# Performance work log

Measured on AMD Instinct MI355X. Metric: run time of the kernel, lower is better.

The kernel has to match this reference:

```python
import jax, jax.numpy as jnp
import numpy as np

N = 4096   # nodes
D = 512    # feature dim
E = 65536  # edges
HOPS = 10  # APPNP K (init arg 'hops')
ALPHA = 0.5


def setup_inputs() -> dict:
    key = jax.random.key(0)
    k1, k2, k3 = jax.random.split(key, 3)
    x_train = jax.random.normal(k1, (N, D), dtype=jnp.float32)
    # kernel_scale = nn.Linear(D, 1, bias=False) weight, flattened to [D]
    w = jax.random.normal(k2, (D,), dtype=jnp.float32) * 0.05
    edge_index = jax.random.randint(k3, (2, E), 0, N, dtype=jnp.int32)
    return {"x_train": x_train, "w": w, "edge_index": edge_index}


def appnp(x0, src, dst, hops, alpha):
    # torch_geometric APPNP with gcn_norm (add self-loops, symmetric norm), dropout=0
    n = x0.shape[0]
    loop = jnp.arange(n, dtype=src.dtype)
    s = jnp.concatenate([src, loop])
    d = jnp.concatenate([dst, loop])
    deg = jax.ops.segment_sum(jnp.ones_like(s, dtype=x0.dtype), d, num_segments=n)
    dis = deg ** -0.5  # deg >= 1 thanks to self-loops
    norm = dis[s] * dis[d]

    def body(h, _):
        agg = jax.ops.segment_sum(norm[:, None] * h[s], d, num_segments=n)
        return (1.0 - alpha) * agg + alpha * x0, None

    h, _ = jax.lax.scan(body, x0, None, length=hops)
    return h


def reference(x_train, w, edge_index):
    n = x_train.shape[0]
    # RBF_kernel: K[i,j] = sum_d w_d * (x_i - x_j)_d^2 for i != j, diag = 1 (the eye)
    xw = x_train * w                                   # [N, D]
    sq = jnp.sum(xw * x_train, axis=1)                 # [N] weighted squared norms
    K = sq[:, None] + sq[None, :] - 2.0 * (xw @ x_train.T)  # [N, N]
    idx = jnp.arange(n)
    K = K.at[idx, idx].set(1.0)

    src, dst = edge_index[0], edge_index[1]
    kgg = appnp(K, src, dst, HOPS, ALPHA)
    kgg = appnp(kgg.T, src, dst, HOPS, ALPHA)

    # adj = dense coo(edge_index, ones); diag = (diag(adj.sum(dim=1)) + 1) ** -0.5
    # (adds 1 to the WHOLE matrix, so off-diagonal entries become 1.0 -- faithful)
    deg_row = jax.ops.segment_sum(jnp.ones((edge_index.shape[1],), K.dtype), src, num_segments=n)
    Dmat = (jnp.diag(deg_row) + 1.0) ** -0.5           # [N, N]
    kgg = Dmat * kgg       # elementwise, as in the original
    kgg = Dmat * kgg.T
    return kgg
```

## Files before the change

### kernel.cpp

```cpp
#include <hip/hip_runtime.h>
#include <stdint.h>

#define Nn 4096
#define Dd 512
#define Ee 65536
#define HOPS 10
#define TPB 512
#define RPT (Nn / TPB)
#define CT 4
#define WCAP 64
#define BCOLS 1028
#define KEXT 1536

typedef unsigned short ushortT;
typedef short bf16x8 __attribute__((ext_vector_type(8)));
typedef float f32x4 __attribute__((ext_vector_type(4)));

__device__ __forceinline__ unsigned short bf16r(float x) {
  unsigned int b = __float_as_uint(x);
  return (unsigned short)((b + 0x7FFFu + ((b >> 16) & 1u)) >> 16);
}
__device__ __forceinline__ float ubf(unsigned short h) {
  return __uint_as_float(((unsigned int)h) << 16);
}
__device__ __forceinline__ void gld16(const unsigned short* g, unsigned short* lds) {
  __builtin_amdgcn_global_load_lds(
      (const __attribute__((address_space(1))) unsigned int*)g,
      (__attribute__((address_space(3))) unsigned int*)lds, 16, 0, 0);
}

__global__ __launch_bounds__(256) void k_sq(const float* __restrict__ x,
                                            const float* __restrict__ w,
                                            float* __restrict__ sq) {
  int row = blockIdx.x;
  int tid = threadIdx.x;
  const float* xr = x + (size_t)row * Dd;
  float partial = 0.f;
  for (int d = tid; d < Dd; d += 256) {
    float xv = xr[d];
    partial += xv * xv * w[d];
  }
  for (int off = 32; off >= 1; off >>= 1) partial += __shfl_down(partial, off, 64);
  __shared__ float red[4];
  int wv = tid >> 6, ln = tid & 63;
  if (ln == 0) red[wv] = partial;
  __syncthreads();
  if (tid == 0) sq[row] = red[0] + red[1] + red[2] + red[3];
}

__global__ void k_count(const int* __restrict__ src, const int* __restrict__ dst,
                        int* __restrict__ degi, int* __restrict__ degrow) {
  int e = blockIdx.x * blockDim.x + threadIdx.x;
  if (e < Ee) {
    atomicAdd(&degi[dst[e]], 1);
    atomicAdd(&degrow[src[e]], 1);
  }
}

__global__ void k_dis(const int* __restrict__ degi, const int* __restrict__ degrow,
                      float* __restrict__ dis, float* __restrict__ d2) {
  int i = blockIdx.x * 256 + threadIdx.x;
  dis[i] = rsqrtf((float)(degi[i] + 1));
  d2[i] = 1.0f / ((float)degrow[i] + 1.0f);
}

__global__ void k_hist(const int* __restrict__ degi, int* __restrict__ binbase) {
  __shared__ int h[WCAP + 1];
  int t = threadIdx.x;
  if (t <= WCAP) h[t] = 0;
  __syncthreads();
  for (int i = t; i < Nn; i += 256) {
    int d = degi[i] + 1;
    if (d > WCAP) d = WCAP;
    atomicAdd(&h[d], 1);
  }
  __syncthreads();
  if (t == 0) {
    int run = 0;
    for (int b = 0; b <= WCAP; b++) { int c = h[b]; binbase[b] = run; run += c; }
  }
}

__global__ void k_scatter(const int* __restrict__ degi, const int* __restrict__ binbase,
                          int* __restrict__ bincnt, int* __restrict__ perm,
                          int* __restrict__ rnk) {
  int i = blockIdx.x * 256 + threadIdx.x;
  int d = degi[i] + 1;
  if (d > WCAP) d = WCAP;
  int pos = binbase[d] + atomicAdd(&bincnt[d], 1);
  perm[pos] = i;
  rnk[i] = pos;
}

__global__ void k_wsub(const int* __restrict__ degi, const int* __restrict__ perm,
                       int* __restrict__ wsub) {
  int t = threadIdx.x;
  int d = degi[perm[t * 64 + 63]] + 1;
  wsub[t] = d > WCAP ? WCAP : d;
}

__global__ void k_fill_ell(const int* __restrict__ src, const int* __restrict__ dst,
                           const float* __restrict__ dis, const int* __restrict__ rnk,
                           int* __restrict__ slot, int2* __restrict__ ell) {
  int i = blockIdx.x * blockDim.x + threadIdx.x;
  if (i < Ee) {
    int s = src[i], d = dst[i];
    int p = atomicAdd(&slot[d], 1);
    if (p < WCAP) ell[(size_t)p * Nn + rnk[d]] = make_int2(s, __float_as_int(dis[s] * dis[d]));
  } else if (i < Ee + Nn) {
    int v = i - Ee;
    int p = atomicAdd(&slot[v], 1);
    if (p < WCAP) ell[(size_t)p * Nn + rnk[v]] = make_int2(v, __float_as_int(dis[v] * dis[v]));
  }
}

__global__ __launch_bounds__(256) void k_xpose(const float* __restrict__ x,
                                               const float* __restrict__ w,
                                               float* __restrict__ xcat) {
  __shared__ float tile[32][33];
  int cx = blockIdx.x, rx = blockIdx.y;
  int t = threadIdx.x, txc = t & 31, tyc = t >> 5;
#pragma unroll
  for (int i = 0; i < 4; i++) {
    int a = tyc + i * 8;
    tile[a][txc] = x[(size_t)(rx * 32 + a) * Dd + cx * 32 + txc];
  }
  __syncthreads();
#pragma unroll
  for (int i = 0; i < 4; i++) {
    int a = tyc + i * 8;
    int c = cx * 32 + a;
    float v = tile[txc][a];
    xcat[(size_t)c * Nn + rx * 32 + txc] = -2.0f * w[c] * v;
    xcat[(size_t)(512 + c) * Nn + rx * 32 + txc] = v;
  }
}

__global__ void k_tail(const float* __restrict__ sq, float* __restrict__ xcat) {
  int r = blockIdx.x * 256 + threadIdx.x;
  xcat[(size_t)1024 * Nn + r] = sq[r];
  xcat[(size_t)1025 * Nn + r] = 1.0f;
  xcat[(size_t)1026 * Nn + r] = 0.0f;
  xcat[(size_t)1027 * Nn + r] = 0.0f;
}

template <int MODE>
__global__ __launch_bounds__(TPB, 4) void k_appnp(const float* __restrict__ xsrc,
                                                  unsigned short* __restrict__ mb,
                                                  unsigned short* __restrict__ aext,
                                                  unsigned short* __restrict__ bext,
                                                  float* __restrict__ mu,
                                                  float* __restrict__ m1,
                                                  const int2* __restrict__ ell,
                                                  const int* __restrict__ perm,
                                                  const int* __restrict__ wsub) {
  extern __shared__ float4 h4[];
  int j0 = blockIdx.x * CT;
  int tid = threadIdx.x;
  int wv = tid >> 6, ln = tid & 63;
  int qb = wv * 512 + ln;

#pragma unroll
  for (int rr = 0; rr < RPT; rr++) {
    int r = tid + rr * TPB;
    float4 v;
    if (MODE == 1) {
      v.x = (r == j0 + 0) ? 1.f : 0.f;
      v.y = (r == j0 + 1) ? 1.f : 0.f;
      v.z = (r == j0 + 2) ? 1.f : 0.f;
      v.w = (r == j0 + 3) ? 1.f : 0.f;
    } else {
      v.x = xsrc[(size_t)(j0 + 0) * Nn + r];
      v.y = xsrc[(size_t)(j0 + 1) * Nn + r];
      v.z = xsrc[(size_t)(j0 + 2) * Nn + r];
      v.w = xsrc[(size_t)(j0 + 3) * Nn + r];
    }
    h4[r] = v;
  }

  int ws[RPT];
#pragma unroll
  for (int rr = 0; rr < RPT; rr++)
    ws[rr] = __builtin_amdgcn_readfirstlane(wsub[wv * 8 + rr]);
  const int Wv = ws[RPT - 1];

  int rp[RPT];
#pragma unroll
  for (int rr = 0; rr < RPT; rr++) rp[rr] = perm[qb + rr * 64];

  __syncthreads();
  float4 x0r[RPT];
#pragma unroll
  for (int rr = 0; rr < RPT; rr++) x0r[rr] = h4[rp[rr]];

  float4 acc[RPT];
  for (int it = 0; it < HOPS; it++) {
    int2 cur[RPT];
#pragma unroll
    for (int rr = 0; rr < RPT; rr++) cur[rr] = ell[qb + rr * 64];
#pragma unroll
    for (int rr = 0; rr < RPT; rr++) acc[rr] = x0r[rr];
    for (int s = 0; s < Wv; s++) {
      int sn = s + 1;
      int2 nxt[RPT];
#pragma unroll
      for (int rr = 0; rr < RPT; rr++)
        if (sn < ws[rr]) nxt[rr] = ell[(size_t)sn * Nn + qb + rr * 64];
#pragma unroll
      for (int rr = 0; rr < RPT; rr++)
        if (s < ws[rr]) {
          float vv = __int_as_float(cur[rr].y);
          float4 hu = h4[cur[rr].x];
          acc[rr].x = fmaf(vv, hu.x, acc[rr].x);
          acc[rr].y = fmaf(vv, hu.y, acc[rr].y);
          acc[rr].z = fmaf(vv, hu.z, acc[rr].z);
          acc[rr].w = fmaf(vv, hu.w, acc[rr].w);
        }
#pragma unroll
      for (int rr = 0; rr < RPT; rr++)
        if (sn < ws[rr]) cur[rr] = nxt[rr];
    }
#pragma unroll
    for (int rr = 0; rr < RPT; rr++) {
      acc[rr].x *= 0.5f; acc[rr].y *= 0.5f; acc[rr].z *= 0.5f; acc[rr].w *= 0.5f;
    }
    __syncthreads();
#pragma unroll
    for (int rr = 0; rr < RPT; rr++) h4[rp[rr]] = acc[rr];
    __syncthreads();
  }

  if (MODE == 1) {
#pragma unroll
    for (int rr = 0; rr < RPT; rr++) {
      int r = tid + rr * TPB;
      float4 a = h4[r];
      ushort4 o = make_ushort4(bf16r(a.x), bf16r(a.y), bf16r(a.z), bf16r(a.w));
      *(ushort4*)&mb[(size_t)r * Nn + j0] = o;
    }
  } else {
    if (j0 < 1024) {
#pragma unroll
      for (int rr = 0; rr < RPT; rr++) {
        int r = tid + rr * TPB;
        float4 a = h4[r];
        ushort4 hi = make_ushort4(bf16r(a.x), bf16r(a.y), bf16r(a.z), bf16r(a.w));
        ushort4 lo = make_ushort4(bf16r(a.x - ubf(hi.x)), bf16r(a.y - ubf(hi.y)),
                                  bf16r(a.z - ubf(hi.z)), bf16r(a.w - ubf(hi.w)));
        if (j0 < 512) {
          *(ushort4*)&aext[(size_t)r * KEXT + j0] = hi;
          *(ushort4*)&aext[(size_t)r * KEXT + 512 + j0] = hi;
          *(ushort4*)&aext[(size_t)r * KEXT + 1024 + j0] = lo;
        } else {
          int c = j0 - 512;
          *(ushort4*)&bext[(size_t)r * KEXT + c] = hi;
          *(ushort4*)&bext[(size_t)r * KEXT + 512 + c] = lo;
          *(ushort4*)&bext[(size_t)r * KEXT + 1024 + c] = hi;
        }
      }
    } else if (j0 == 1024) {
#pragma unroll
      for (int rr = 0; rr < RPT; rr++) {
        int r = tid + rr * TPB;
        float4 a = h4[r];
        mu[r] = a.x;
        m1[r] = a.y;
      }
    }
  }
}

__device__ __forceinline__ void mm_step(const unsigned short* __restrict__ Ap, int lda,
                                        const unsigned short* __restrict__ Bp, int ldb,
                                        unsigned short* As, unsigned short* Bs,
                                        int i0, int j0, int k0, int l, int w, int wr,
                                        int wc, f32x4 acc[4][4]) {
#pragma unroll
  for (int j = 0; j < 2; j++) {
    int row = (w * 2 + j) * 16 + (l >> 2);
    int clog = (l & 3) ^ ((row >> 1) & 3);
    gld16(Ap + (size_t)(i0 + row) * lda + k0 + clog * 8, As + (w * 2 + j) * 512);
    gld16(Bp + (size_t)(j0 + row) * ldb + k0 + clog * 8, Bs + (w * 2 + j) * 512);
  }
  __syncthreads();
  bf16x8 af[4], bg[4];
#pragma unroll
  for (int m = 0; m < 4; m++) {
    int ar = wr * 64 + m * 16 + (l & 15);
    af[m] = *(const bf16x8*)(As + ar * 32 + (((l >> 4) ^ ((ar >> 1) & 3))) * 8);
    int br = wc * 64 + m * 16 + (l & 15);
    bg[m] = *(const bf16x8*)(Bs + br * 32 + (((l >> 4) ^ ((br >> 1) & 3))) * 8);
  }
#pragma unroll
  for (int m = 0; m < 4; m++)
#pragma unroll
    for (int n = 0; n < 4; n++)
      acc[m][n] = __builtin_amdgcn_mfma_f32_16x16x32_bf16(af[m], bg[n], acc[m][n], 0, 0, 0);
  __syncthreads();
}

__global__ __launch_bounds__(256) void k_mm(const unsigned short* __restrict__ Mb,
                                            const unsigned short* __restrict__ Aext,
                                            const unsigned short* __restrict__ Bext,
                                            const float* __restrict__ mu,
                                            const float* __restrict__ m1,
                                            const float* __restrict__ d2,
                                            float* __restrict__ out) {
  __shared__ unsigned short As[128 * 32];
  __shared__ unsigned short Bs[128 * 32];
  int i0 = blockIdx.y * 128, j0 = blockIdx.x * 128;
  int tid = threadIdx.x, l = tid & 63, w = tid >> 6;
  int wr = w >> 1, wc = w & 1;
  f32x4 acc[4][4];
#pragma unroll
  for (int m = 0; m < 4; m++)
#pragma unroll
    for (int n = 0; n < 4; n++) acc[m][n] = (f32x4){0.f, 0.f, 0.f, 0.f};

  for (int k0 = 0; k0 < Nn; k0 += 32)
    mm_step(Mb, Nn, Mb, Nn, As, Bs, i0, j0, k0, l, w, wr, wc, acc);
  for (int k0 = 0; k0 < KEXT; k0 += 32)
    mm_step(Aext, KEXT, Bext, KEXT, As, Bs, i0, j0, k0, l, w, wr, wc, acc);

#pragma unroll
  for (int m = 0; m < 4; m++) {
#pragma unroll
    for (int n = 0; n < 4; n++) {
#pragma unroll
      for (int q = 0; q < 4; q++) {
        int gi = i0 + wr * 64 + m * 16 + ((l >> 4) << 2) + q;
        int gj = j0 + wc * 64 + n * 16 + (l & 15);
        float v = acc[m][n][q] + mu[gi] * m1[gj] + m1[gi] * mu[gj];
        if (gi == gj) v *= d2[gi];
        out[(size_t)gi * Nn + gj] = v;
      }
    }
  }
}

extern "C" void kernel_launch(void* const* d_in, const int* in_sizes, int n_in,
                              void* d_out, int out_size, void* d_ws, size_t ws_size,
                              hipStream_t stream) {
  const float* x = (const float*)d_in[0];
  const float* w = (const float*)d_in[1];
  const int* ei = (const int*)d_in[2];
  const int* src = ei;
  const int* dstv = ei + Ee;
  float* out = (float*)d_out;

  unsigned short* Mb = (unsigned short*)d_ws;
  float* xcat = (float*)d_ws;
  unsigned short* aext = (unsigned short*)((char*)d_ws + (size_t)Nn * Nn * 2);
  unsigned short* bext = aext + (size_t)Nn * KEXT;
  int2* ell = (int2*)(bext + (size_t)Nn * KEXT);
  float* sq = (float*)(ell + (size_t)WCAP * Nn);
  float* dis = sq + Nn;
  float* d2 = dis + Nn;
  float* mu = d2 + Nn;
  float* m1 = mu + Nn;
  int* degi = (int*)(m1 + Nn);
  int* degrow = degi + Nn;
  int* slotcnt = degrow + Nn;
  int* bincnt = slotcnt + Nn;
  int* binbase = bincnt + (WCAP + 1);
  int* perm = binbase + (WCAP + 1);
  int* rnk = perm + Nn;
  int* wsub = rnk + Nn;

  hipMemsetAsync(ell, 0, (size_t)WCAP * Nn * sizeof(int2), stream);
  hipMemsetAsync(degi, 0, sizeof(int) * (3 * Nn + (WCAP + 1)), stream);

  k_sq<<<Nn, 256, 0, stream>>>(x, w, sq);
  k_count<<<Ee / 256, 256, 0, stream>>>(src, dstv, degi, degrow);
  k_dis<<<Nn / 256, 256, 0, stream>>>(degi, degrow, dis, d2);
  k_hist<<<1, 256, 0, stream>>>(degi, binbase);
  k_scatter<<<Nn / 256, 256, 0, stream>>>(degi, binbase, bincnt, perm, rnk);
  k_wsub<<<1, 64, 0, stream>>>(degi, perm, wsub);
  k_fill_ell<<<(Ee + Nn + 255) / 256, 256, 0, stream>>>(src, dstv, dis, rnk, slotcnt, ell);
  k_xpose<<<dim3(16, 128), 256, 0, stream>>>(x, w, xcat);
  k_tail<<<Nn / 256, 256, 0, stream>>>(sq, xcat);

  k_appnp<0><<<BCOLS / CT, TPB, Nn * sizeof(float4), stream>>>(xcat, nullptr, aext, bext, mu,
                                                               m1, ell, perm, wsub);
  k_appnp<1><<<Nn / CT, TPB, Nn * sizeof(float4), stream>>>(nullptr, Mb, nullptr, nullptr,
                                                            nullptr, nullptr, ell, perm, wsub);
  k_mm<<<dim3(Nn / 128, Nn / 128), 256, 0, stream>>>(Mb, aext, bext, mu, m1, d2, out);
}
```

Baseline: 1.041 ms.

## Propagate x once and apply weights after APPNP; widen GEMM K-tile and swizzle blocks

The APPNP propagation is linear, so propagating the -2*w*x columns is replaced by propagating x alone and scaling by -2*w after propagation. This halves the number of feature columns diffused (516 instead of 1028). The final GEMM also moves from a K-step of 32 to 64 with a new XOR-swizzled LDS layout, which halves the number of barriers per K. Block indices are remapped so neighbouring workgroups share tiles in cache. The cost is more LDS per block (32KB), which may lower occupancy, and slightly different rounding from scaling after propagation.

```diff
diff --git a/kernel.cpp b/kernel.cpp
--- a/kernel.cpp
+++ b/kernel.cpp
@@ -9,10 +9,9 @@
 #define RPT (Nn / TPB)
 #define CT 4
 #define WCAP 64
-#define BCOLS 1028
+#define BCOLS 516
 #define KEXT 1536
 
-typedef unsigned short ushortT;
 typedef short bf16x8 __attribute__((ext_vector_type(8)));
 typedef float f32x4 __attribute__((ext_vector_type(4)));
 
@@ -115,7 +114,6 @@
 }
 
 __global__ __launch_bounds__(256) void k_xpose(const float* __restrict__ x,
-                                               const float* __restrict__ w,
                                                float* __restrict__ xcat) {
   __shared__ float tile[32][33];
   int cx = blockIdx.x, rx = blockIdx.y;
@@ -130,22 +128,21 @@
   for (int i = 0; i < 4; i++) {
     int a = tyc + i * 8;
     int c = cx * 32 + a;
-    float v = tile[txc][a];
-    xcat[(size_t)c * Nn + rx * 32 + txc] = -2.0f * w[c] * v;
-    xcat[(size_t)(512 + c) * Nn + rx * 32 + txc] = v;
+    xcat[(size_t)c * Nn + rx * 32 + txc] = tile[txc][a];
   }
 }
 
 __global__ void k_tail(const float* __restrict__ sq, float* __restrict__ xcat) {
   int r = blockIdx.x * 256 + threadIdx.x;
-  xcat[(size_t)1024 * Nn + r] = sq[r];
-  xcat[(size_t)1025 * Nn + r] = 1.0f;
-  xcat[(size_t)1026 * Nn + r] = 0.0f;
-  xcat[(size_t)1027 * Nn + r] = 0.0f;
+  xcat[(size_t)512 * Nn + r] = sq[r];
+  xcat[(size_t)513 * Nn + r] = 1.0f;
+  xcat[(size_t)514 * Nn + r] = 0.0f;
+  xcat[(size_t)515 * Nn + r] = 0.0f;
 }
 
 template <int MODE>
 __global__ __launch_bounds__(TPB, 4) void k_appnp(const float* __restrict__ xsrc,
+                                                  const float* __restrict__ wp,
                                                   unsigned short* __restrict__ mb,
                                                   unsigned short* __restrict__ aext,
                                                   unsigned short* __restrict__ bext,
@@ -239,26 +236,28 @@
       *(ushort4*)&mb[(size_t)r * Nn + j0] = o;
     }
   } else {
-    if (j0 < 1024) {
+    if (j0 < 512) {
+      float w0 = -2.f * wp[j0 + 0], w1 = -2.f * wp[j0 + 1];
+      float w2 = -2.f * wp[j0 + 2], w3 = -2.f * wp[j0 + 3];
 #pragma unroll
       for (int rr = 0; rr < RPT; rr++) {
         int r = tid + rr * TPB;
         float4 a = h4[r];
-        ushort4 hi = make_ushort4(bf16r(a.x), bf16r(a.y), bf16r(a.z), bf16r(a.w));
-        ushort4 lo = make_ushort4(bf16r(a.x - ubf(hi.x)), bf16r(a.y - ubf(hi.y)),
-                                  bf16r(a.z - ubf(hi.z)), bf16r(a.w - ubf(hi.w)));
-        if (j0 < 512) {
-          *(ushort4*)&aext[(size_t)r * KEXT + j0] = hi;
-          *(ushort4*)&aext[(size_t)r * KEXT + 512 + j0] = hi;
-          *(ushort4*)&aext[(size_t)r * KEXT + 1024 + j0] = lo;
-        } else {
-          int c = j0 - 512;
-          *(ushort4*)&bext[(size_t)r * KEXT + c] = hi;
-          *(ushort4*)&bext[(size_t)r * KEXT + 512 + c] = lo;
-          *(ushort4*)&bext[(size_t)r * KEXT + 1024 + c] = hi;
-        }
+        ushort4 yhi = make_ushort4(bf16r(a.x), bf16r(a.y), bf16r(a.z), bf16r(a.w));
+        ushort4 ylo = make_ushort4(bf16r(a.x - ubf(yhi.x)), bf16r(a.y - ubf(yhi.y)),
+                                   bf16r(a.z - ubf(yhi.z)), bf16r(a.w - ubf(yhi.w)));
+        float4 p = make_float4(w0 * a.x, w1 * a.y, w2 * a.z, w3 * a.w);
+        ushort4 phi = make_ushort4(bf16r(p.x), bf16r(p.y), bf16r(p.z), bf16r(p.w));
+        ushort4 plo = make_ushort4(bf16r(p.x - ubf(phi.x)), bf16r(p.y - ubf(phi.y)),
+                                   bf16r(p.z - ubf(phi.z)), bf16r(p.w - ubf(phi.w)));
+        *(ushort4*)&bext[(size_t)r * KEXT + j0] = yhi;
+        *(ushort4*)&bext[(size_t)r * KEXT + 512 + j0] = ylo;
+        *(ushort4*)&bext[(size_t)r * KEXT + 1024 + j0] = yhi;
+        *(ushort4*)&aext[(size_t)r * KEXT + j0] = phi;
+        *(ushort4*)&aext[(size_t)r * KEXT + 512 + j0] = phi;
+        *(ushort4*)&aext[(size_t)r * KEXT + 1024 + j0] = plo;
       }
-    } else if (j0 == 1024) {
+    } else if (j0 == 512) {
 #pragma unroll
       for (int rr = 0; rr < RPT; rr++) {
         int r = tid + rr * TPB;
@@ -275,27 +274,31 @@
                                         unsigned short* As, unsigned short* Bs,
                                         int i0, int j0, int k0, int l, int w, int wr,
                                         int wc, f32x4 acc[4][4]) {
-#pragma unroll
-  for (int j = 0; j < 2; j++) {
-    int row = (w * 2 + j) * 16 + (l >> 2);
-    int clog = (l & 3) ^ ((row >> 1) & 3);
-    gld16(Ap + (size_t)(i0 + row) * lda + k0 + clog * 8, As + (w * 2 + j) * 512);
-    gld16(Bp + (size_t)(j0 + row) * ldb + k0 + clog * 8, Bs + (w * 2 + j) * 512);
-  }
-  __syncthreads();
-  bf16x8 af[4], bg[4];
-#pragma unroll
-  for (int m = 0; m < 4; m++) {
-    int ar = wr * 64 + m * 16 + (l & 15);
-    af[m] = *(const bf16x8*)(As + ar * 32 + (((l >> 4) ^ ((ar >> 1) & 3))) * 8);
-    int br = wc * 64 + m * 16 + (l & 15);
-    bg[m] = *(const bf16x8*)(Bs + br * 32 + (((l >> 4) ^ ((br >> 1) & 3))) * 8);
-  }
-#pragma unroll
-  for (int m = 0; m < 4; m++)
-#pragma unroll
-    for (int n = 0; n < 4; n++)
-      acc[m][n] = __builtin_amdgcn_mfma_f32_16x16x32_bf16(af[m], bg[n], acc[m][n], 0, 0, 0);
+  int rsub = w * 8 + (l >> 3);
+  int scg = ((l & 7) ^ (l >> 3)) * 8;
+#pragma unroll
+  for (int r = 0; r < 4; r++) {
+    int row = r * 32 + rsub;
+    gld16(Ap + (size_t)(i0 + row) * lda + k0 + scg, As + (r * 32 + w * 8) * 64);
+    gld16(Bp + (size_t)(j0 + row) * ldb + k0 + scg, Bs + (r * 32 + w * 8) * 64);
+  }
+  __syncthreads();
+#pragma unroll
+  for (int q = 0; q < 2; q++) {
+    bf16x8 af[4], bg[4];
+#pragma unroll
+    for (int m = 0; m < 4; m++) {
+      int ar = wr * 64 + m * 16 + (l & 15);
+      af[m] = *(const bf16x8*)(As + ar * 64 + ((((l >> 4) + 4 * q) ^ (ar & 7)) * 8));
+      int br = wc * 64 + m * 16 + (l & 15);
+      bg[m] = *(const bf16x8*)(Bs + br * 64 + ((((l >> 4) + 4 * q) ^ (br & 7)) * 8));
+    }
+#pragma unroll
+    for (int m = 0; m < 4; m++)
+#pragma unroll
+      for (int n = 0; n < 4; n++)
+        acc[m][n] = __builtin_amdgcn_mfma_f32_16x16x32_bf16(af[m], bg[n], acc[m][n], 0, 0, 0);
+  }
   __syncthreads();
 }
 
@@ -306,9 +309,11 @@
                                             const float* __restrict__ m1,
                                             const float* __restrict__ d2,
                                             float* __restrict__ out) {
-  __shared__ unsigned short As[128 * 32];
-  __shared__ unsigned short Bs[128 * 32];
-  int i0 = blockIdx.y * 128, j0 = blockIdx.x * 128;
+  __shared__ unsigned short As[128 * 64];
+  __shared__ unsigned short Bs[128 * 64];
+  int lid = blockIdx.y * 32 + blockIdx.x;
+  int swz = (lid & 7) * 128 + (lid >> 3);
+  int i0 = (swz >> 5) * 128, j0 = (swz & 31) * 128;
   int tid = threadIdx.x, l = tid & 63, w = tid >> 6;
   int wr = w >> 1, wc = w & 1;
   f32x4 acc[4][4];
@@ -317,9 +322,9 @@
 #pragma unroll
     for (int n = 0; n < 4; n++) acc[m][n] = (f32x4){0.f, 0.f, 0.f, 0.f};
 
-  for (int k0 = 0; k0 < Nn; k0 += 32)
+  for (int k0 = 0; k0 < Nn; k0 += 64)
     mm_step(Mb, Nn, Mb, Nn, As, Bs, i0, j0, k0, l, w, wr, wc, acc);
-  for (int k0 = 0; k0 < KEXT; k0 += 32)
+  for (int k0 = 0; k0 < KEXT; k0 += 64)
     mm_step(Aext, KEXT, Bext, KEXT, As, Bs, i0, j0, k0, l, w, wr, wc, acc);
 
 #pragma unroll
@@ -377,12 +382,13 @@
   k_scatter<<<Nn / 256, 256, 0, stream>>>(degi, binbase, bincnt, perm, rnk);
   k_wsub<<<1, 64, 0, stream>>>(degi, perm, wsub);
   k_fill_ell<<<(Ee + Nn + 255) / 256, 256, 0, stream>>>(src, dstv, dis, rnk, slotcnt, ell);
-  k_xpose<<<dim3(16, 128), 256, 0, stream>>>(x, w, xcat);
+  k_xpose<<<dim3(16, 128), 256, 0, stream>>>(x, xcat);
   k_tail<<<Nn / 256, 256, 0, stream>>>(sq, xcat);
 
-  k_appnp<0><<<BCOLS / CT, TPB, Nn * sizeof(float4), stream>>>(xcat, nullptr, aext, bext, mu,
-                                                               m1, ell, perm, wsub);
-  k_appnp<1><<<Nn / CT, TPB, Nn * sizeof(float4), stream>>>(nullptr, Mb, nullptr, nullptr,
-                                                            nullptr, nullptr, ell, perm, wsub);
-  k_mm<<<dim3(Nn / 128, Nn / 128), 256, 0, stream>>>(Mb, aext, bext, mu, m1, d2, out);
-}
+  k_appnp<0><<<BCOLS / CT, TPB, Nn * sizeof(float4), stream>>>(xcat, w, nullptr, aext, bext,
+                                                               mu, m1, ell, perm, wsub);
+  k_appnp<1><<<Nn / CT, TPB, Nn * sizeof(float4), stream>>>(nullptr, nullptr, Mb, nullptr,
+                                                            nullptr, nullptr, nullptr, ell,
+                                                            perm, wsub);
+  k_mm<<<dim3(32, 32), 256, 0, stream>>>(Mb, aext, bext, mu, m1, d2, out);
+}
```

Result: faster. 971.7 us (-6.6%).
